# Optimization experiments

Hardware: AMD Instinct MI355X
Metric: run time of the kernel (lower is better)

The kernel has to match this reference:

```python
import jax, jax.numpy as jnp
import numpy as np

H = 12
D_K = 64
NEG = -1e9
EPS = 1e-6
SQRT_2_PI = float(np.sqrt(2.0 / np.pi))


def gelu_tanh(x):
    return 0.5 * x * (1.0 + jnp.tanh(SQRT_2_PI * (x + 0.044715 * x * x * x)))


def layernorm(x, a, b):
    # torch std is unbiased (ddof=1); note original adds eps to std, not var
    mean = jnp.mean(x, axis=-1, keepdims=True)
    n = x.shape[-1]
    var = jnp.sum((x - mean) ** 2, axis=-1, keepdims=True) / (n - 1)
    std = jnp.sqrt(var)
    return a * (x - mean) / (std + EPS) + b


def setup_inputs() -> dict:
    key = jax.random.key(0)
    ks = jax.random.split(key, 16)
    B, S, D, F = 8, 1024, 768, 3072
    s = 0.02
    inp = {
        "x": jax.random.normal(ks[0], (B, S, D), jnp.float32),
        "mask": jnp.ones((B, 1, 1, S), jnp.int32),
        "Wq": jax.random.normal(ks[1], (D, D), jnp.float32) * s,
        "bq": jnp.zeros((D,), jnp.float32),
        "Wk": jax.random.normal(ks[2], (D, D), jnp.float32) * s,
        "bk": jnp.zeros((D,), jnp.float32),
        "Wv": jax.random.normal(ks[3], (D, D), jnp.float32) * s,
        "bv": jnp.zeros((D,), jnp.float32),
        "Wo": jax.random.normal(ks[4], (D, D), jnp.float32) * s,
        "bo": jnp.zeros((D,), jnp.float32),
        "W1": jax.random.normal(ks[5], (D, F), jnp.float32) * s,
        "b1": jnp.zeros((F,), jnp.float32),
        "W2": jax.random.normal(ks[6], (F, D), jnp.float32) * s,
        "b2": jnp.zeros((D,), jnp.float32),
        "ln1_a": jnp.ones((D,), jnp.float32),
        "ln1_b": jnp.ones((D,), jnp.float32),
        "ln2_a": jnp.ones((D,), jnp.float32),
        "ln2_b": jnp.ones((D,), jnp.float32),
    }
    return inp


def reference(x, mask, Wq, bq, Wk, bk, Wv, bv, Wo, bo, W1, b1, W2, b2,
              ln1_a, ln1_b, ln2_a, ln2_b):
    B, S, D = x.shape
    # QKV projections -> [B, H, S, d_k]
    def split_heads(t):
        return t.reshape(B, S, H, D_K).transpose(0, 2, 1, 3)
    q = split_heads(x @ Wq + bq)
    k = split_heads(x @ Wk + bk)
    v = split_heads(x @ Wv + bv)
    scores = jnp.einsum("bhqd,bhkd->bhqk", q, k) / jnp.sqrt(jnp.float32(D_K))
    scores = jnp.where(mask == 0, jnp.float32(NEG), scores)
    p = jax.nn.softmax(scores, axis=-1)
    attn = jnp.einsum("bhqk,bhkd->bhqd", p, v)
    attn = attn.transpose(0, 2, 1, 3).reshape(B, S, D)
    attn_out = attn @ Wo + bo
    out1 = layernorm(x + attn_out, ln1_a, ln1_b)
    ffn = gelu_tanh(out1 @ W1 + b1) @ W2 + b2
    out2 = layernorm(out1 + ffn, ln2_a, ln2_b)
    return out2
```

## Files before the change

### kernel.cpp

```cpp
#include <hip/hip_runtime.h>
#include <hip/hip_bf16.h>
#include <math.h>

#define BB 8
#define SS 1024
#define DD 768
#define FF 3072
#define HH 12
#define DK 64

typedef __bf16 bf16;
typedef __attribute__((ext_vector_type(8))) __bf16 bf16x8;
typedef __attribute__((ext_vector_type(4))) __bf16 bf16x4;
typedef __attribute__((ext_vector_type(4))) float f32x4;

#define AS1 __attribute__((address_space(1)))
#define AS3 __attribute__((address_space(3)))

#define EXP2_SCALE 0.18033688011112042f
#define NLOG2E2    -2.8853900817779268f
#define MASK_BIAS  -1.8033688e8f

__device__ __forceinline__ float gelu_fast(float x) {
    const float u = 0.7978845608028654f * (x + 0.044715f * x * x * x);
    const float e = __builtin_amdgcn_exp2f(u * NLOG2E2);
    return x * __builtin_amdgcn_rcpf(1.0f + e);
}

template<int BN, int BK, int OUTB, int GELU_F, int RESID, int VT, int RB16>
__global__ __launch_bounds__(256) void gemm_bf16(
    const bf16* __restrict__ A, const bf16* __restrict__ Bt,
    const float* __restrict__ bias, const void* __restrict__ R,
    void* __restrict__ Cout, bf16* __restrict__ Vt, int M, int N, int K)
{
    constexpr int NTJ = BN / 32;
    constexpr int CPR = BK / 8;
    constexpr int AR  = 128 * CPR / 256;
    constexpr int BR  = BN * CPR / 256;
    constexpr int KS  = BK / 32;

    __shared__ bf16x8 As[128 * CPR];
    __shared__ bf16x8 Bs[BN * CPR];

    const int t    = threadIdx.x;
    const int wave = t >> 6;
    const int lane = t & 63;
    const int mtiles = M >> 7;
    const int m0 = (blockIdx.x % mtiles) * 128;
    const int n0 = (blockIdx.x / mtiles) * BN;
    const int wm = (wave >> 1) * 64;
    const int wn = (wave & 1) * (BN / 2);
    const int col  = lane & 15;
    const int quad = lane >> 4;

    f32x4 acc[4][NTJ] = {};

    const bf16* Abase = A  + (size_t)m0 * K;
    const bf16* Bbase = Bt + (size_t)n0 * K;

    for (int k0 = 0; k0 < K; k0 += BK) {
        if (k0) __syncthreads();

        #pragma unroll
        for (int i = 0; i < AR; ++i) {
            const int chunk = i * 256 + wave * 64 + lane;
            const int r  = chunk / CPR;
            const int kc = (chunk & (CPR - 1)) ^ (r & (CPR - 1));
            const bf16* ga = Abase + (size_t)r * K + k0 + kc * 8;
            __builtin_amdgcn_global_load_lds((AS1 void*)ga, (AS3 void*)(As + i * 256 + wave * 64), 16, 0, 0);
        }
        #pragma unroll
        for (int i = 0; i < BR; ++i) {
            const int chunk = i * 256 + wave * 64 + lane;
            const int r  = chunk / CPR;
            const int kc = (chunk & (CPR - 1)) ^ (r & (CPR - 1));
            const bf16* gb = Bbase + (size_t)r * K + k0 + kc * 8;
            __builtin_amdgcn_global_load_lds((AS1 void*)gb, (AS3 void*)(Bs + i * 256 + wave * 64), 16, 0, 0);
        }
        __syncthreads();

        const bf16* Asp = (const bf16*)As;
        const bf16* Bsp = (const bf16*)Bs;
        #pragma unroll
        for (int ks = 0; ks < KS; ++ks) {
            bf16x8 af[4], bfr[NTJ];
            #pragma unroll
            for (int ti = 0; ti < 4; ++ti) {
                const int r  = wm + ti * 16 + col;
                const int cs = (ks * 4 + quad) ^ (r & (CPR - 1));
                af[ti] = *(const bf16x8*)(Asp + r * BK + cs * 8);
            }
            #pragma unroll
            for (int tj = 0; tj < NTJ; ++tj) {
                const int r  = wn + tj * 16 + col;
                const int cs = (ks * 4 + quad) ^ (r & (CPR - 1));
                bfr[tj] = *(const bf16x8*)(Bsp + r * BK + cs * 8);
            }
            #pragma unroll
            for (int ti = 0; ti < 4; ++ti)
                #pragma unroll
                for (int tj = 0; tj < NTJ; ++tj)
                    acc[ti][tj] = __builtin_amdgcn_mfma_f32_16x16x32_bf16(
                        af[ti], bfr[tj], acc[ti][tj], 0, 0, 0);
        }
    }

    float biasv[NTJ];
    #pragma unroll
    for (int tj = 0; tj < NTJ; ++tj) biasv[tj] = bias[n0 + wn + tj * 16 + col];

    #pragma unroll
    for (int ti = 0; ti < 4; ++ti) {
        #pragma unroll
        for (int tj = 0; tj < NTJ; ++tj) {
            const int n = n0 + wn + tj * 16 + col;
            const bool vcol = VT && (n >= 2 * DD);
            if (VT && vcol) {
                const int hh = (n - 2 * DD) >> 6;
                const int dd = (n - 2 * DD) & 63;
                const int mb = m0 + wm + ti * 16 + quad * 4;
                const int bb = mb >> 10, ss0 = mb & 1023;
                bf16x4 pk;
                #pragma unroll
                for (int i = 0; i < 4; ++i)
                    pk[i] = (bf16)(acc[ti][tj][i] + biasv[tj]);
                *(bf16x4*)(Vt + (size_t)((bb * HH + hh) * DK + dd) * SS + ss0) = pk;
            } else {
                #pragma unroll
                for (int i = 0; i < 4; ++i) {
                    const int m = m0 + wm + ti * 16 + quad * 4 + i;
                    float v = acc[ti][tj][i] + biasv[tj];
                    if (GELU_F) v = gelu_fast(v);
                    if (RESID) {
                        if (RB16) v += (float)((const bf16*)R)[(size_t)m * N + n];
                        else      v += ((const float*)R)[(size_t)m * N + n];
                    }
                    if (OUTB) ((bf16*)Cout)[(size_t)m * N + n] = (bf16)v;
                    else      ((float*)Cout)[(size_t)m * N + n] = v;
                }
            }
        }
    }
}

__device__ __forceinline__ void tc32(
    const float* __restrict__ src, bf16* __restrict__ dst,
    int R, int C, int c0, int r0, int t)
{
    __shared__ float tile[32][33];
    const int tx = t & 31, ty = t >> 5;
    #pragma unroll
    for (int i = 0; i < 32; i += 8)
        tile[ty + i][tx] = src[(size_t)(r0 + ty + i) * C + c0 + tx];
    __syncthreads();
    #pragma unroll
    for (int i = 0; i < 32; i += 8)
        dst[(size_t)(c0 + ty + i) * R + r0 + tx] = (bf16)tile[tx][ty + i];
}

__global__ __launch_bounds__(256) void prep_all(
    const float* __restrict__ Wq, const float* __restrict__ Wk,
    const float* __restrict__ Wv, const float* __restrict__ Wo,
    const float* __restrict__ W1, const float* __restrict__ W2,
    const float* __restrict__ bq, const float* __restrict__ bk,
    const float* __restrict__ bv, const float* __restrict__ x,
    bf16* __restrict__ wqkvb, bf16* __restrict__ wob,
    bf16* __restrict__ wt1b,  bf16* __restrict__ wt2b,
    float* __restrict__ bqkv, bf16x4* __restrict__ xb)
{
    const int blk = blockIdx.x;
    const int t = threadIdx.x;
    if (blk < 2304) {
        const int job = blk / 576, loc = blk % 576;
        const int c0 = (loc % 24) * 32, r0 = (loc / 24) * 32;
        const float* src = (job == 0) ? Wq : (job == 1) ? Wk : (job == 2) ? Wv : Wo;
        bf16* dst = (job == 3) ? wob : wqkvb + (size_t)job * DD * DD;
        tc32(src, dst, DD, DD, c0, r0, t);
    } else if (blk < 4608) {
        const int loc = blk - 2304;
        tc32(W1, wt1b, DD, FF, (loc % 96) * 32, (loc / 96) * 32, t);
    } else if (blk < 6912) {
        const int loc = blk - 4608;
        tc32(W2, wt2b, FF, DD, (loc % 24) * 32, (loc / 24) * 32, t);
    } else if (blk < 6921) {
        const int i = (blk - 6912) * 256 + t;
        if (i < 3 * DD)
            bqkv[i] = (i < DD) ? bq[i] : (i < 2 * DD ? bk[i - DD] : bv[i - 2 * DD]);
    } else {
        const int i = (blk - 6921) * 256 + t;
        const float4 v = ((const float4*)x)[i];
        bf16x4 o;
        o.x = (bf16)v.x; o.y = (bf16)v.y; o.z = (bf16)v.z; o.w = (bf16)v.w;
        xb[i] = o;
    }
}

__global__ __launch_bounds__(512) void flash_mfma(
    const bf16* __restrict__ qkvb,
    const bf16* __restrict__ vtb,
    const int*  __restrict__ mask,
    bf16* __restrict__ O)
{
    __shared__ bf16x8 Ks[1024];
    __shared__ bf16x8 Vs[1024];
    __shared__ bf16   Ps[8 * 16 * 64];
    __shared__ float  Mb[SS];

    const int t    = threadIdx.x;
    const int wave = t >> 6;
    const int lane = t & 63;
    const int col  = lane & 15;
    const int quad = lane >> 4;
    const int bh = blockIdx.x % (BB * HH);
    const int q0 = (blockIdx.x / (BB * HH)) * 128;
    const int b  = bh / HH;
    const int h  = bh % HH;

    #pragma unroll
    for (int i = 0; i < 2; ++i) {
        const int c = t + i * 512;
        Mb[c] = (mask[b * SS + c] == 0) ? MASK_BIAS : 0.0f;
    }

    bf16x8 aq[2];
    #pragma unroll
    for (int ks = 0; ks < 2; ++ks)
        aq[ks] = *(const bf16x8*)(qkvb
            + (size_t)(b * SS + q0 + wave * 16 + col) * 2304
            + h * DK + ks * 32 + quad * 8);

    f32x4 o[4] = {};
    float l_part[4] = {};

    bf16* Pw = Ps + wave * 1024;

    for (int it = 0; it < SS / 128; ++it) {
        const int c0 = it * 128;
        if (it) __syncthreads();

        #pragma unroll
        for (int i = 0; i < 2; ++i) {
            const int chunk = i * 512 + t;
            const int r  = chunk >> 3;
            const int kc = (chunk & 7) ^ (r & 7);
            const bf16* gk = qkvb + (size_t)(b * SS + c0 + r) * 2304 + DD + h * DK + kc * 8;
            __builtin_amdgcn_global_load_lds((AS1 void*)gk,
                (AS3 void*)(Ks + i * 512 + t), 16, 0, 0);
        }
        #pragma unroll
        for (int i = 0; i < 2; ++i) {
            const int chunk = i * 512 + t;
            const int r  = chunk >> 4;
            const int cc = (chunk & 15) ^ (r & 15);
            const bf16* gv = vtb + (size_t)(bh * DK + r) * SS + c0 + cc * 8;
            __builtin_amdgcn_global_load_lds((AS1 void*)gv,
                (AS3 void*)(Vs + i * 512 + t), 16, 0, 0);
        }
        __syncthreads();

        const bf16* Ksp = (const bf16*)Ks;
        const bf16* Vsp = (const bf16*)Vs;

        #pragma unroll
        for (int ss = 0; ss < 2; ++ss) {
            const int cb = c0 + ss * 64;

            f32x4 s4[4] = {};
            {
                bf16x8 kf[2][4];
                #pragma unroll
                for (int ks = 0; ks < 2; ++ks)
                    #pragma unroll
                    for (int tj = 0; tj < 4; ++tj) {
                        const int r  = ss * 64 + tj * 16 + col;
                        const int sl = (ks * 4 + quad) ^ (r & 7);
                        kf[ks][tj] = *(const bf16x8*)(Ksp + r * 64 + sl * 8);
                    }
                #pragma unroll
                for (int ks = 0; ks < 2; ++ks)
                    #pragma unroll
                    for (int tj = 0; tj < 4; ++tj)
                        s4[tj] = __builtin_amdgcn_mfma_f32_16x16x32_bf16(
                            aq[ks], kf[ks][tj], s4[tj], 0, 0, 0);
            }

            float mbv[4];
            #pragma unroll
            for (int tj = 0; tj < 4; ++tj) mbv[tj] = Mb[cb + tj * 16 + col];

            #pragma unroll
            for (int i = 0; i < 4; ++i) {
                const int rf = quad * 4 + i;
                #pragma unroll
                for (int tj = 0; tj < 4; ++tj) {
                    const float p = __builtin_amdgcn_exp2f(
                        __builtin_fmaf(s4[tj][i], EXP2_SCALE, mbv[tj]));
                    l_part[i] += p;
                    const int c  = tj * 16 + col;
                    const int sl = ((c >> 3) ^ (rf & 7));
                    Pw[rf * 64 + sl * 8 + (c & 7)] = (bf16)p;
                }
            }

            {
                bf16x8 vf[2][4];
                #pragma unroll
                for (int ks = 0; ks < 2; ++ks)
                    #pragma unroll
                    for (int tj = 0; tj < 4; ++tj) {
                        const int r  = tj * 16 + col;
                        const int lc = ss * 8 + ks * 4 + quad;
                        const int sl = lc ^ (r & 15);
                        vf[ks][tj] = *(const bf16x8*)(Vsp + r * 128 + sl * 8);
                    }
                bf16x8 pf[2];
                #pragma unroll
                for (int ks = 0; ks < 2; ++ks) {
                    const int rf = col;
                    const int sl = (ks * 4 + quad) ^ (rf & 7);
                    pf[ks] = *(const bf16x8*)(Pw + rf * 64 + sl * 8);
                }
                #pragma unroll
                for (int ks = 0; ks < 2; ++ks)
                    #pragma unroll
                    for (int tj = 0; tj < 4; ++tj)
                        o[tj] = __builtin_amdgcn_mfma_f32_16x16x32_bf16(
                            pf[ks], vf[ks][tj], o[tj], 0, 0, 0);
            }
        }
    }

    #pragma unroll
    for (int i = 0; i < 4; ++i) {
        float l = l_part[i];
        #pragma unroll
        for (int off = 1; off < 16; off <<= 1)
            l += __shfl_xor(l, off, 64);
        const float inv = 1.0f / l;
        const int q = q0 + wave * 16 + quad * 4 + i;
        #pragma unroll
        for (int tj = 0; tj < 4; ++tj)
            O[(size_t)(b * SS + q) * DD + h * DK + tj * 16 + col] =
                (bf16)(o[tj][i] * inv);
    }
}

template<int IN_B16, int OUTF, int OUTBF>
__global__ __launch_bounds__(256) void layernorm_k(
    const void* __restrict__ X,
    const float* __restrict__ ga, const float* __restrict__ gb,
    float* __restrict__ out, bf16* __restrict__ outb)
{
    __shared__ float red[4];
    const int row = blockIdx.x;
    const int t   = threadIdx.x;

    float v[3];
    #pragma unroll
    for (int i = 0; i < 3; ++i) {
        const int c = t + i * 256;
        if (IN_B16) v[i] = (float)((const bf16*)X)[(size_t)row * DD + c];
        else        v[i] = ((const float*)X)[(size_t)row * DD + c];
    }

    float s = v[0] + v[1] + v[2];
    #pragma unroll
    for (int off = 32; off > 0; off >>= 1) s += __shfl_down(s, off, 64);
    if ((t & 63) == 0) red[t >> 6] = s;
    __syncthreads();
    const float mean = (red[0] + red[1] + red[2] + red[3]) * (1.0f / 768.0f);
    __syncthreads();

    float sq = 0.f;
    #pragma unroll
    for (int i = 0; i < 3; ++i) { const float d = v[i] - mean; sq += d * d; }
    #pragma unroll
    for (int off = 32; off > 0; off >>= 1) sq += __shfl_down(sq, off, 64);
    if ((t & 63) == 0) red[t >> 6] = sq;
    __syncthreads();
    const float var = (red[0] + red[1] + red[2] + red[3]) * (1.0f / 767.0f);
    const float inv = 1.0f / (sqrtf(var) + 1e-6f);

    #pragma unroll
    for (int i = 0; i < 3; ++i) {
        const int c = t + i * 256;
        const float r = ga[c] * (v[i] - mean) * inv + gb[c];
        if (OUTF)  out[(size_t)row * DD + c] = r;
        if (OUTBF) outb[(size_t)row * DD + c] = (bf16)r;
    }
}

extern "C" void kernel_launch(void* const* d_in, const int* in_sizes, int n_in,
                              void* d_out, int out_size, void* d_ws, size_t ws_size,
                              hipStream_t stream)
{
    const float* x    = (const float*)d_in[0];
    const int*   mask = (const int*)  d_in[1];
    const float* Wq   = (const float*)d_in[2];
    const float* bq   = (const float*)d_in[3];
    const float* Wk   = (const float*)d_in[4];
    const float* bk   = (const float*)d_in[5];
    const float* Wv   = (const float*)d_in[6];
    const float* bv   = (const float*)d_in[7];
    const float* Wo   = (const float*)d_in[8];
    const float* bo   = (const float*)d_in[9];
    const float* W1   = (const float*)d_in[10];
    const float* b1   = (const float*)d_in[11];
    const float* W2   = (const float*)d_in[12];
    const float* b2   = (const float*)d_in[13];
    const float* ln1a = (const float*)d_in[14];
    const float* ln1b = (const float*)d_in[15];
    const float* ln2a = (const float*)d_in[16];
    const float* ln2b = (const float*)d_in[17];
    float* out = (float*)d_out;

    const int M = BB * SS;
    const size_t nBSD = (size_t)M * DD;

    char* w = (char*)d_ws;
    bf16*  qkvb  = (bf16*)w;            w += (size_t)M * 3 * DD * 2;
    bf16*  vtb   = (bf16*)w;            w += (size_t)BB * HH * DK * SS * 2;
    bf16*  attnb = (bf16*)w;            w += nBSD * 2;
    bf16*  attn_sum = (bf16*)w;         w += nBSD * 2;
    bf16*  ffn_sum = (bf16*)w;          w += nBSD * 2;
    bf16*  xb    = (bf16*)w;            w += nBSD * 2;
    bf16*  hbuf  = (bf16*)w;            w += (size_t)M * FF * 2;
    bf16*  wqkvb = (bf16*)w;            w += (size_t)3 * DD * DD * 2;
    bf16*  wob   = (bf16*)w;            w += (size_t)DD * DD * 2;
    bf16*  wt1b  = (bf16*)w;            w += (size_t)DD * FF * 2;
    bf16*  wt2b  = (bf16*)w;            w += (size_t)FF * DD * 2;
    float* bqkv  = (float*)w;           w += (size_t)3 * DD * 4;
    bf16*  out1b = xb;

    const dim3 blk(256);

    prep_all<<<dim3(13065), blk, 0, stream>>>(
        Wq, Wk, Wv, Wo, W1, W2, bq, bk, bv, x,
        wqkvb, wob, wt1b, wt2b, bqkv, (bf16x4*)xb);

    gemm_bf16<128, 64, 1, 0, 0, 1, 0><<<dim3((M / 128) * (3 * DD / 128)), blk, 0, stream>>>(
        xb, wqkvb, bqkv, nullptr, qkvb, vtb, M, 3 * DD, DD);

    flash_mfma<<<dim3((SS / 128) * BB * HH), dim3(512), 0, stream>>>(
        qkvb, vtb, mask, attnb);

    gemm_bf16<64, 128, 1, 0, 1, 0, 1><<<dim3((M / 128) * (DD / 64)), blk, 0, stream>>>(
        attnb, wob, bo, xb, attn_sum, nullptr, M, DD, DD);

    layernorm_k<1, 0, 1><<<dim3(M), blk, 0, stream>>>(
        attn_sum, ln1a, ln1b, nullptr, out1b);

    gemm_bf16<128, 64, 1, 1, 0, 0, 0><<<dim3((M / 128) * (FF / 128)), blk, 0, stream>>>(
        out1b, wt1b, b1, nullptr, hbuf, nullptr, M, FF, DD);

    gemm_bf16<64, 128, 1, 0, 1, 0, 1><<<dim3((M / 128) * (DD / 64)), blk, 0, stream>>>(
        hbuf, wt2b, b2, out1b, ffn_sum, nullptr, M, DD, FF);

    layernorm_k<1, 1, 0><<<dim3(M), blk, 0, stream>>>(
        ffn_sum, ln2a, ln2b, out, nullptr);
}
```

Baseline: 333.0 us.

## Add 8-wave 128x64 GEMM kernel for Wo and W2 projections

Adds a dedicated GEMM kernel with 512 threads (8 waves, each computing a 32x32 sub-tile) over a 128x64 output tile with K-step 128, using XOR-swizzled direct global-to-LDS loads. It replaces the 256-thread templated GEMM for the two N=768 projections (attention output and FFN down) that include a residual add. The aim is more waves per tile for these narrow-N GEMMs, giving better latency hiding and MFMA occupancy. The tradeoff is that each wave does less MFMA work per LDS read, and there is no double buffering, so every K step waits on its loads.

```diff
diff --git a/kernel.cpp b/kernel.cpp
--- a/kernel.cpp
+++ b/kernel.cpp
@@ -141,6 +141,96 @@
             }
         }
     }
+}
+
+__global__ __launch_bounds__(512) void gemm64_w8(
+    const bf16* __restrict__ A, const bf16* __restrict__ Bt,
+    const float* __restrict__ bias, const bf16* __restrict__ R,
+    bf16* __restrict__ Cout, int M, int N, int K)
+{
+    __shared__ bf16x8 As[2048];
+    __shared__ bf16x8 Bs[1024];
+
+    const int t    = threadIdx.x;
+    const int wave = t >> 6;
+    const int lane = t & 63;
+    const int mtiles = M >> 7;
+    const int m0 = (blockIdx.x % mtiles) * 128;
+    const int n0 = (blockIdx.x / mtiles) * 64;
+    const int wm = (wave >> 1) * 32;
+    const int wn = (wave & 1) * 32;
+    const int col  = lane & 15;
+    const int quad = lane >> 4;
+
+    f32x4 acc[2][2] = {};
+
+    const bf16* Abase = A  + (size_t)m0 * K;
+    const bf16* Bbase = Bt + (size_t)n0 * K;
+
+    for (int k0 = 0; k0 < K; k0 += 128) {
+        if (k0) __syncthreads();
+
+        #pragma unroll
+        for (int i = 0; i < 4; ++i) {
+            const int chunk = i * 512 + t;
+            const int r  = chunk >> 4;
+            const int kc = (chunk & 15) ^ (r & 15);
+            const bf16* ga = Abase + (size_t)r * K + k0 + kc * 8;
+            __builtin_amdgcn_global_load_lds((AS1 void*)ga, (AS3 void*)(As + i * 512 + t), 16, 0, 0);
+        }
+        #pragma unroll
+        for (int i = 0; i < 2; ++i) {
+            const int chunk = i * 512 + t;
+            const int r  = chunk >> 4;
+            const int kc = (chunk & 15) ^ (r & 15);
+            const bf16* gb = Bbase + (size_t)r * K + k0 + kc * 8;
+            __builtin_amdgcn_global_load_lds((AS1 void*)gb, (AS3 void*)(Bs + i * 512 + t), 16, 0, 0);
+        }
+        __syncthreads();
+
+        const bf16* Asp = (const bf16*)As;
+        const bf16* Bsp = (const bf16*)Bs;
+        #pragma unroll
+        for (int ks = 0; ks < 4; ++ks) {
+            bf16x8 af[2], bfr[2];
+            #pragma unroll
+            for (int ti = 0; ti < 2; ++ti) {
+                const int r  = wm + ti * 16 + col;
+                const int cs = (ks * 4 + quad) ^ (r & 15);
+                af[ti] = *(const bf16x8*)(Asp + r * 128 + cs * 8);
+            }
+            #pragma unroll
+            for (int tj = 0; tj < 2; ++tj) {
+                const int r  = wn + tj * 16 + col;
+                const int cs = (ks * 4 + quad) ^ (r & 15);
+                bfr[tj] = *(const bf16x8*)(Bsp + r * 128 + cs * 8);
+            }
+            #pragma unroll
+            for (int ti = 0; ti < 2; ++ti)
+                #pragma unroll
+                for (int tj = 0; tj < 2; ++tj)
+                    acc[ti][tj] = __builtin_amdgcn_mfma_f32_16x16x32_bf16(
+                        af[ti], bfr[tj], acc[ti][tj], 0, 0, 0);
+        }
+    }
+
+    float biasv[2];
+    #pragma unroll
+    for (int tj = 0; tj < 2; ++tj) biasv[tj] = bias[n0 + wn + tj * 16 + col];
+
+    #pragma unroll
+    for (int ti = 0; ti < 2; ++ti)
+        #pragma unroll
+        for (int tj = 0; tj < 2; ++tj) {
+            const int n = n0 + wn + tj * 16 + col;
+            #pragma unroll
+            for (int i = 0; i < 4; ++i) {
+                const int m = m0 + wm + ti * 16 + quad * 4 + i;
+                const float v = acc[ti][tj][i] + biasv[tj]
+                              + (float)R[(size_t)m * N + n];
+                Cout[(size_t)m * N + n] = (bf16)v;
+            }
+        }
 }
 
 __device__ __forceinline__ void tc32(
@@ -444,8 +534,8 @@
     flash_mfma<<<dim3((SS / 128) * BB * HH), dim3(512), 0, stream>>>(
         qkvb, vtb, mask, attnb);
 
-    gemm_bf16<64, 128, 1, 0, 1, 0, 1><<<dim3((M / 128) * (DD / 64)), blk, 0, stream>>>(
-        attnb, wob, bo, xb, attn_sum, nullptr, M, DD, DD);
+    gemm64_w8<<<dim3((M / 128) * (DD / 64)), dim3(512), 0, stream>>>(
+        attnb, wob, bo, xb, attn_sum, M, DD, DD);
 
     layernorm_k<1, 0, 1><<<dim3(M), blk, 0, stream>>>(
         attn_sum, ln1a, ln1b, nullptr, out1b);
@@ -453,8 +543,8 @@
     gemm_bf16<128, 64, 1, 1, 0, 0, 0><<<dim3((M / 128) * (FF / 128)), blk, 0, stream>>>(
         out1b, wt1b, b1, nullptr, hbuf, nullptr, M, FF, DD);
 
-    gemm_bf16<64, 128, 1, 0, 1, 0, 1><<<dim3((M / 128) * (DD / 64)), blk, 0, stream>>>(
-        hbuf, wt2b, b2, out1b, ffn_sum, nullptr, M, DD, FF);
+    gemm64_w8<<<dim3((M / 128) * (DD / 64)), dim3(512), 0, stream>>>(
+        hbuf, wt2b, b2, out1b, ffn_sum, M, DD, FF);
 
     layernorm_k<1, 1, 0><<<dim3(M), blk, 0, stream>>>(
         ffn_sum, ln2a, ln2b, out, nullptr);
```

New measurement: 359.1 us. 1.08x slower.
